# Performance work log

Measured on AMD Instinct MI355X. Metric: run time of the kernel, lower is better.

The kernel has to match this reference:

```python
import jax, jax.numpy as jnp
import numpy as np

N = 100000
E = 1600000
IN_C = 128
OUT_C = 64
HID = 2 * OUT_C  # 128


def setup_inputs() -> dict:
    key = jax.random.key(0)
    ks = jax.random.split(key, 10)
    s = lambda fan_in: 1.0 / np.sqrt(fan_in)
    inp = {
        "x": jax.random.normal(ks[0], (N, IN_C), dtype=jnp.float32),
        "edge_index": jax.random.randint(ks[1], (2, E), 0, N, dtype=jnp.int64),
        # SAGEConv params: lin_l acts on aggregated neighbors (with bias), lin_r on root (no bias)
        "W1l": jax.random.uniform(ks[2], (IN_C, HID), jnp.float32, -s(IN_C), s(IN_C)),
        "b1": jnp.zeros((HID,), jnp.float32),
        "W1r": jax.random.uniform(ks[3], (IN_C, HID), jnp.float32, -s(IN_C), s(IN_C)),
        "Wml": jax.random.uniform(ks[4], (HID, OUT_C), jnp.float32, -s(HID), s(HID)),
        "bm": jnp.zeros((OUT_C,), jnp.float32),
        "Wmr": jax.random.uniform(ks[5], (HID, OUT_C), jnp.float32, -s(HID), s(HID)),
        "Wsl": jax.random.uniform(ks[6], (HID, OUT_C), jnp.float32, -s(HID), s(HID)),
        "bs": jnp.zeros((OUT_C,), jnp.float32),
        "Wsr": jax.random.uniform(ks[7], (HID, OUT_C), jnp.float32, -s(HID), s(HID)),
    }
    return inp


def _sage_mean(x, src, dst, Wl, b, Wr):
    n = x.shape[0]
    # mean aggregation of source features onto destination nodes
    agg = jax.ops.segment_sum(x[src], dst, num_segments=n)
    cnt = jax.ops.segment_sum(jnp.ones((src.shape[0],), x.dtype), dst, num_segments=n)
    agg = agg / jnp.maximum(cnt, 1.0)[:, None]
    return agg @ Wl + b + x @ Wr


def reference(x, edge_index, W1l, b1, W1r, Wml, bm, Wmr, Wsl, bs, Wsr):
    src, dst = edge_index[0], edge_index[1]
    h = jax.nn.relu(_sage_mean(x, src, dst, W1l, b1, W1r))
    mu = _sage_mean(h, src, dst, Wml, bm, Wmr)
    logstd = _sage_mean(h, src, dst, Wsl, bs, Wsr)
    return mu, logstd
```

## Files before the change

kernel.cpp:

```cpp
#include <hip/hip_runtime.h>


typedef __attribute__((ext_vector_type(8))) short bf16x8;
typedef __attribute__((ext_vector_type(4))) float f32x4;
typedef __attribute__((ext_vector_type(2))) float f32x2;

#define SHIFT 9
#define BW 512

__device__ __forceinline__ unsigned short f2bf(float f) {
    unsigned u = __builtin_bit_cast(unsigned, f);
    u += 0x7fff + ((u >> 16) & 1);
    return (unsigned short)(u >> 16);
}
__device__ __forceinline__ float bflo(unsigned u) { return __builtin_bit_cast(float, u << 16); }
__device__ __forceinline__ float bfhi(unsigned u) { return __builtin_bit_cast(float, u & 0xffff0000u); }

__global__ __launch_bounds__(256) void prep_kernel(
    const float* __restrict__ x, const int* __restrict__ raw, int* __restrict__ flag,
    const float* __restrict__ W1l, const float* __restrict__ W1r,
    const float* __restrict__ Wml, const float* __restrict__ Wmr,
    const float* __restrict__ Wsl, const float* __restrict__ Wsr,
    const float* __restrict__ bm, const float* __restrict__ bs,
    unsigned short* __restrict__ B1p, unsigned short* __restrict__ B2p,
    float* __restrict__ bc, unsigned short* __restrict__ A1,
    unsigned short* __restrict__ A2, int n, int nE, int nXB) {
    const int b = blockIdx.x;
    const int t = threadIdx.x;
    if (b < nXB) {
        int i = (b * 256 + t) * 4;
        if (i < n * 128) {
            float4 v = *reinterpret_cast<const float4*>(x + i);
            int row = i >> 7, col = i & 127;
            unsigned short* p = A1 + (size_t)row * 256 + 128 + col;
            p[0] = f2bf(v.x); p[1] = f2bf(v.y); p[2] = f2bf(v.z); p[3] = f2bf(v.w);
        }
    } else if (b < nXB + 64) {
        const int nCheck = nE < 65536 ? nE : 65536;
        int acc = 0;
        for (int i = (b - nXB) * 256 + t; i < nCheck; i += 64 * 256)
            acc |= raw[2 * i + 1];
        if (acc) atomicOr(flag, 1);
    } else if (b < nXB + 192) {
        int i = (b - nXB - 64) * 256 + t;
        int j = i & 7, lq = (i >> 3) & 63, ks = (i >> 9) & 7, nf = i >> 12;
        int k = ks * 32 + (lq >> 4) * 8 + j;
        int c = nf * 16 + (lq & 15);
        float w1 = (k < 128) ? W1l[k * 128 + c] : W1r[(k - 128) * 128 + c];
        float w2;
        if (k < 128) w2 = (c < 64) ? Wml[k * 64 + c] : Wsl[k * 64 + (c - 64)];
        else         w2 = (c < 64) ? Wmr[(k - 128) * 64 + c] : Wsr[(k - 128) * 64 + (c - 64)];
        B1p[i] = f2bf(w1);
        B2p[i] = f2bf(w2);
        if (i < 128) bc[i] = (i < 64) ? bm[i] : bs[i - 64];
    } else {
        if (t < 64) {
            ((unsigned*)A1)[(size_t)n * 128 + 64 + t] = 0;
            ((unsigned*)A2)[(size_t)n * 128 + 64 + t] = 0;
        }
    }
}

__global__ __launch_bounds__(256) void binA_kernel(
    const int* __restrict__ raw, const int* __restrict__ flag,
    int* __restrict__ bcnt, unsigned* __restrict__ recs, int nE, int cap) {
    __shared__ int cnt[256];
    __shared__ int gbase[256];
    const int t = threadIdx.x;
    const bool is64 = (flag[0] == 0);
    const long long base = (long long)blockIdx.x * 1024;
    cnt[t] = 0;
    __syncthreads();
    int packv[4], loff[4], bk[4];
#pragma unroll
    for (int k = 0; k < 4; ++k) {
        long long e = base + t + k * 256;
        bk[k] = -1;
        if (e < nE) {
            int s, d;
            if (is64) { s = raw[2 * e]; d = raw[2 * (nE + e)]; }
            else      { s = raw[e];     d = raw[nE + e]; }
            bk[k] = d >> SHIFT;
            packv[k] = (s << SHIFT) | (d & (BW - 1));
            loff[k] = atomicAdd(&cnt[bk[k]], 1);
        }
    }
    __syncthreads();
    {
        int c = cnt[t];
        gbase[t] = c ? atomicAdd(&bcnt[t], c) : 0;
    }
    __syncthreads();
#pragma unroll
    for (int k = 0; k < 4; ++k) {
        if (bk[k] >= 0) {
            int pos = gbase[bk[k]] + loff[k];
            if (pos < cap) recs[(size_t)bk[k] * cap + pos] = (unsigned)packv[k];
        }
    }
}

__global__ __launch_bounds__(256) void binB_kernel(
    const unsigned* __restrict__ recs, const int* __restrict__ bcnt,
    int* __restrict__ rowptrP, int* __restrict__ cnts,
    int* __restrict__ csr, int cap, int n, int NB) {
    __shared__ int sdeg[BW];
    __shared__ int scur[BW];
    __shared__ int ssum[256];
    const int b = blockIdx.x;
    const int t = threadIdx.x;
    const int node0 = b << SHIFT;

    int rawb = (t < NB) ? bcnt[t] : 0;
    ssum[t] = rawb;
    __syncthreads();
    for (int off = 1; off < 256; off <<= 1) {
        int val = (t >= off) ? ssum[t - off] : 0;
        __syncthreads();
        ssum[t] += val;
        __syncthreads();
    }
    const int base = ((b == 0) ? 0 : ssum[b - 1]) + b * 3 * BW;
    int cnt = bcnt[b];
    if (cnt > cap) cnt = cap;
    const unsigned* r = recs + (size_t)b * cap;
    __syncthreads();

    sdeg[t] = 0;
    sdeg[t + 256] = 0;
    __syncthreads();
    for (int i = t; i < cnt; i += 256) atomicAdd(&sdeg[r[i] & (BW - 1)], 1);
    __syncthreads();
    int d0 = sdeg[2 * t], d1 = sdeg[2 * t + 1];
    int p0 = (d0 + 3) & ~3, p1 = (d1 + 3) & ~3;
    int sum = p0 + p1;
    ssum[t] = sum;
    __syncthreads();
    for (int off = 1; off < 256; off <<= 1) {
        int val = (t >= off) ? ssum[t - off] : 0;
        __syncthreads();
        ssum[t] += val;
        __syncthreads();
    }
    int ex = ssum[t] - sum;
    scur[2 * t] = ex;
    scur[2 * t + 1] = ex + p0;
    __syncthreads();
#pragma unroll
    for (int q = 0; q < 2; ++q) {
        int i = 2 * t + q;
        int node = node0 + i;
        if (node < n) {
            rowptrP[node] = base + scur[i];
            cnts[node] = sdeg[i];
        }
    }
    __syncthreads();
    for (int i = t; i < cnt; i += 256) {
        unsigned rec = r[i];
        int pos = base + atomicAdd(&scur[rec & (BW - 1)], 1);
        csr[pos] = (int)(rec >> SHIFT);
    }
    __syncthreads();
#pragma unroll
    for (int q = 0; q < 2; ++q) {
        int i = 2 * t + q;
        int node = node0 + i;
        if (node < n) {
            int d = sdeg[i];
            int pad = (4 - (d & 3)) & 3;
            int st = base + scur[i];
            for (int k = 0; k < pad; ++k) csr[st + k] = n;
        }
    }
}

__global__ __launch_bounds__(256) void gather_kernel(const unsigned int* __restrict__ feat,
                                                     const int* __restrict__ rowptrP,
                                                     const int* __restrict__ cnts,
                                                     const int* __restrict__ csr,
                                                     unsigned int* __restrict__ agg, int n) {
    int wv = (blockIdx.x * 256 + threadIdx.x) >> 6;
    if (wv >= n) return;
    int lane = threadIdx.x & 63;
    int eg = lane >> 4;
    int c4 = (lane & 15) * 4;
    int beg = rowptrP[wv];
    int deg = cnts[wv];
    int endp = beg + ((deg + 3) & ~3);
    f32x2 a0 = (f32x2)(0.f), a1 = (f32x2)(0.f), a2 = (f32x2)(0.f), a3 = (f32x2)(0.f);
    int jb = beg;
    if (jb < endp) {
        int s = csr[jb + eg];
        uint4 v = *reinterpret_cast<const uint4*>(feat + (size_t)s * 128 + c4);
#pragma unroll 2
        for (jb += 4; jb < endp; jb += 4) {
            int s2 = csr[jb + eg];
            uint4 v2 = *reinterpret_cast<const uint4*>(feat + (size_t)s2 * 128 + c4);
            a0 += (f32x2){bflo(v.x), bfhi(v.x)};
            a1 += (f32x2){bflo(v.y), bfhi(v.y)};
            a2 += (f32x2){bflo(v.z), bfhi(v.z)};
            a3 += (f32x2){bflo(v.w), bfhi(v.w)};
            v = v2;
        }
        a0 += (f32x2){bflo(v.x), bfhi(v.x)};
        a1 += (f32x2){bflo(v.y), bfhi(v.y)};
        a2 += (f32x2){bflo(v.z), bfhi(v.z)};
        a3 += (f32x2){bflo(v.w), bfhi(v.w)};
    }
    float acc[8] = {a0.x, a0.y, a1.x, a1.y, a2.x, a2.y, a3.x, a3.y};
#pragma unroll
    for (int q = 0; q < 8; ++q) {
        acc[q] += __shfl_xor(acc[q], 16);
        acc[q] += __shfl_xor(acc[q], 32);
    }
    if (eg == 0) {
        float ic = 1.0f / fmaxf((float)deg, 1.0f);
        uint4 r;
        r.x = (unsigned)f2bf(acc[0] * ic) | ((unsigned)f2bf(acc[1] * ic) << 16);
        r.y = (unsigned)f2bf(acc[2] * ic) | ((unsigned)f2bf(acc[3] * ic) << 16);
        r.z = (unsigned)f2bf(acc[4] * ic) | ((unsigned)f2bf(acc[5] * ic) << 16);
        r.w = (unsigned)f2bf(acc[6] * ic) | ((unsigned)f2bf(acc[7] * ic) << 16);
        *reinterpret_cast<uint4*>(agg + (size_t)wv * 128 + c4) = r;
    }
}

template <int MODE>
__global__ __launch_bounds__(256) void mfma_gemm(const unsigned short* __restrict__ A,
                                                 const unsigned short* __restrict__ Bp,
                                                 const float* __restrict__ bias,
                                                 void* __restrict__ outp, int n) {
    const int tid = threadIdx.x;
    const int w = tid >> 6, l = tid & 63;
    const int lr = l & 15;
    const int lg = l >> 4;
    const int row0 = blockIdx.x * 128 + w * 32;

    f32x4 acc[2][8];
#pragma unroll
    for (int mf = 0; mf < 2; ++mf)
#pragma unroll
        for (int nf = 0; nf < 8; ++nf) acc[mf][nf] = (f32x4)(0.0f);

    int r0 = row0 + lr;       if (r0 > n - 1) r0 = n - 1;
    int r1 = row0 + 16 + lr;  if (r1 > n - 1) r1 = n - 1;
    const unsigned short* a0p = A + (size_t)r0 * 256 + lg * 8;
    const unsigned short* a1p = A + (size_t)r1 * 256 + lg * 8;
    const unsigned short* bp = Bp + (size_t)l * 8;

    for (int ks = 0; ks < 8; ++ks) {
        bf16x8 a0 = *reinterpret_cast<const bf16x8*>(a0p + ks * 32);
        bf16x8 a1 = *reinterpret_cast<const bf16x8*>(a1p + ks * 32);
#pragma unroll
        for (int nf = 0; nf < 8; ++nf) {
            bf16x8 b = *reinterpret_cast<const bf16x8*>(bp + ((nf * 8 + ks) << 9));
            acc[0][nf] = __builtin_amdgcn_mfma_f32_16x16x32_bf16(a0, b, acc[0][nf], 0, 0, 0);
            acc[1][nf] = __builtin_amdgcn_mfma_f32_16x16x32_bf16(a1, b, acc[1][nf], 0, 0, 0);
        }
    }

    float bv[8];
#pragma unroll
    for (int nf = 0; nf < 8; ++nf) bv[nf] = bias[nf * 16 + lr];

#pragma unroll
    for (int mf = 0; mf < 2; ++mf)
#pragma unroll
        for (int j = 0; j < 4; ++j) {
            int row = row0 + mf * 16 + lg * 4 + j;
            if (row >= n) continue;
#pragma unroll
            for (int nf = 0; nf < 8; ++nf) {
                int col = nf * 16 + lr;
                float v = acc[mf][nf][j] + bv[nf];
                if (MODE == 0) {
                    v = fmaxf(v, 0.0f);
                    ((unsigned short*)outp)[(size_t)row * 256 + 128 + col] = f2bf(v);
                } else {
                    float* o = (float*)outp;
                    if (col < 64) o[(size_t)row * 64 + col] = v;
                    else o[(size_t)n * 64 + (size_t)row * 64 + (col - 64)] = v;
                }
            }
        }
}

extern "C" void kernel_launch(void* const* d_in, const int* in_sizes, int n_in,
                              void* d_out, int out_size, void* d_ws, size_t ws_size,
                              hipStream_t stream) {
    const float* x = (const float*)d_in[0];
    const int* eidx_raw = (const int*)d_in[1];
    const float* W1l = (const float*)d_in[2];
    const float* b1 = (const float*)d_in[3];
    const float* W1r = (const float*)d_in[4];
    const float* Wml = (const float*)d_in[5];
    const float* bm = (const float*)d_in[6];
    const float* Wmr = (const float*)d_in[7];
    const float* Wsl = (const float*)d_in[8];
    const float* bs = (const float*)d_in[9];
    const float* Wsr = (const float*)d_in[10];
    float* out = (float*)d_out;

    const int n = in_sizes[0] / 128;
    const int nE = in_sizes[1] / 2;

    const int NB = ((n - 1) >> SHIFT) + 1;
    long long capll = (((long long)nE << SHIFT) / n) * 5 / 4 + 1024;
    const int cap = (int)((capll + 15) & ~15LL);
    const int csr_ints = nE + NB * 3 * BW + 64;

    char* ws = (char*)d_ws;
    const size_t a_bytes = (size_t)(n + 1) * 512;
    const size_t a1_off = 0;
    const size_t a2_off = a1_off + a_bytes;
    const size_t recs_off = a2_off;
    const size_t csr_off = a2_off + a_bytes;
    const size_t rowptr_off = csr_off + (size_t)csr_ints * 4;
    const size_t cnts_off = rowptr_off + (size_t)n * 4;
    const size_t bcnt_off = cnts_off + (size_t)n * 4;
    const size_t flag_off = bcnt_off + 1024;
    const size_t b1p_off = (flag_off + 4 + 255) & ~(size_t)255;
    const size_t b2p_off = b1p_off + 65536;
    const size_t bc_off = b2p_off + 65536;

    unsigned short* A1 = (unsigned short*)(ws + a1_off);
    unsigned short* A2 = (unsigned short*)(ws + a2_off);
    unsigned* recs = (unsigned*)(ws + recs_off);
    int* csr = (int*)(ws + csr_off);
    int* rowptrP = (int*)(ws + rowptr_off);
    int* cnts = (int*)(ws + cnts_off);
    int* bcnt = (int*)(ws + bcnt_off);
    int* flag = (int*)(ws + flag_off);
    unsigned short* B1p = (unsigned short*)(ws + b1p_off);
    unsigned short* B2p = (unsigned short*)(ws + b2p_off);
    float* bc = (float*)(ws + bc_off);

    hipMemsetAsync(bcnt, 0, 1024 + 4, stream);

    const int nXB = (n * 32 + 255) / 256;
    prep_kernel<<<nXB + 193, 256, 0, stream>>>(x, eidx_raw, flag, W1l, W1r, Wml, Wmr,
                                               Wsl, Wsr, bm, bs, B1p, B2p, bc, A1, A2,
                                               n, nE, nXB);

    binA_kernel<<<(nE + 1023) / 1024, 256, 0, stream>>>(eidx_raw, flag, bcnt, recs, nE, cap);
    binB_kernel<<<NB, 256, 0, stream>>>(recs, bcnt, rowptrP, cnts, csr, cap, n, NB);

    const int gather_blocks = (n * 64 + 255) / 256;
    const int gemm_blocks = (n + 127) / 128;

    gather_kernel<<<gather_blocks, 256, 0, stream>>>(
        (const unsigned int*)A1 + 64, rowptrP, cnts, csr, (unsigned int*)A1, n);
    mfma_gemm<0><<<gemm_blocks, 256, 0, stream>>>(A1, B1p, b1, A2, n);

    gather_kernel<<<gather_blocks, 256, 0, stream>>>(
        (const unsigned int*)A2 + 64, rowptrP, cnts, csr, (unsigned int*)A2, n);
    mfma_gemm<1><<<gemm_blocks, 256, 0, stream>>>(A2, B2p, bc, out, n);
}
```

Before: 287.9 us.

## Fuse edge binning into prep kernel with per-block dtype check; prefetch gather indices

Merges the prep and binA kernels into one launch. Each binning block detects int64 vs int32 edge indices on its own, so the global flag and its memory dependency go away. Binning now runs in two passes (count, then scatter) over 4096 edges per block, which rereads the edge data. The gather loop also prefetches the next CSR index one iteration ahead to shorten the dependent-load chain.

```diff
diff --git a/kernel.cpp b/kernel.cpp
--- a/kernel.cpp
+++ b/kernel.cpp
@@ -16,33 +16,60 @@
 __device__ __forceinline__ float bflo(unsigned u) { return __builtin_bit_cast(float, u << 16); }
 __device__ __forceinline__ float bfhi(unsigned u) { return __builtin_bit_cast(float, u & 0xffff0000u); }
 
-__global__ __launch_bounds__(256) void prep_kernel(
-    const float* __restrict__ x, const int* __restrict__ raw, int* __restrict__ flag,
+__global__ __launch_bounds__(256) void stage1_kernel(
+    const float* __restrict__ x, const int* __restrict__ raw,
     const float* __restrict__ W1l, const float* __restrict__ W1r,
     const float* __restrict__ Wml, const float* __restrict__ Wmr,
     const float* __restrict__ Wsl, const float* __restrict__ Wsr,
     const float* __restrict__ bm, const float* __restrict__ bs,
     unsigned short* __restrict__ B1p, unsigned short* __restrict__ B2p,
     float* __restrict__ bc, unsigned short* __restrict__ A1,
-    unsigned short* __restrict__ A2, int n, int nE, int nXB) {
+    unsigned short* __restrict__ A2, int* __restrict__ bcnt,
+    unsigned* __restrict__ recs, int n, int nE, int cap, int nBinA, int nXB) {
     const int b = blockIdx.x;
     const int t = threadIdx.x;
-    if (b < nXB) {
-        int i = (b * 256 + t) * 4;
+    if (b < nBinA) {
+        __shared__ int cnt[256];
+        __shared__ int cur[256];
+        __shared__ int gbase[256];
+        __shared__ int sflag;
+        const int e0 = b * 4096;
+        const int e1 = (e0 + 4096 < nE) ? e0 + 4096 : nE;
+        int acc = 0;
+        for (int e = e0 + t; e < e1; e += 256) acc |= raw[2 * e + 1];
+        if (t == 0) sflag = 0;
+        cnt[t] = 0;
+        cur[t] = 0;
+        __syncthreads();
+        if (acc) atomicOr(&sflag, 1);
+        __syncthreads();
+        const bool is64 = (sflag == 0);
+        for (int e = e0 + t; e < e1; e += 256) {
+            int d = is64 ? raw[2 * (nE + e)] : raw[nE + e];
+            atomicAdd(&cnt[d >> SHIFT], 1);
+        }
+        __syncthreads();
+        gbase[t] = cnt[t] ? atomicAdd(&bcnt[t], cnt[t]) : 0;
+        __syncthreads();
+        for (int e = e0 + t; e < e1; e += 256) {
+            int s, d;
+            if (is64) { s = raw[2 * e]; d = raw[2 * (nE + e)]; }
+            else      { s = raw[e];     d = raw[nE + e]; }
+            int bk = d >> SHIFT;
+            int pos = gbase[bk] + atomicAdd(&cur[bk], 1);
+            if (pos < cap)
+                recs[(size_t)bk * cap + pos] = ((unsigned)s << SHIFT) | (unsigned)(d & (BW - 1));
+        }
+    } else if (b < nBinA + nXB) {
+        int i = ((b - nBinA) * 256 + t) * 4;
         if (i < n * 128) {
             float4 v = *reinterpret_cast<const float4*>(x + i);
             int row = i >> 7, col = i & 127;
             unsigned short* p = A1 + (size_t)row * 256 + 128 + col;
             p[0] = f2bf(v.x); p[1] = f2bf(v.y); p[2] = f2bf(v.z); p[3] = f2bf(v.w);
         }
-    } else if (b < nXB + 64) {
-        const int nCheck = nE < 65536 ? nE : 65536;
-        int acc = 0;
-        for (int i = (b - nXB) * 256 + t; i < nCheck; i += 64 * 256)
-            acc |= raw[2 * i + 1];
-        if (acc) atomicOr(flag, 1);
-    } else if (b < nXB + 192) {
-        int i = (b - nXB - 64) * 256 + t;
+    } else if (b < nBinA + nXB + 128) {
+        int i = (b - nBinA - nXB) * 256 + t;
         int j = i & 7, lq = (i >> 3) & 63, ks = (i >> 9) & 7, nf = i >> 12;
         int k = ks * 32 + (lq >> 4) * 8 + j;
         int c = nf * 16 + (lq & 15);
@@ -61,45 +88,6 @@
     }
 }
 
-__global__ __launch_bounds__(256) void binA_kernel(
-    const int* __restrict__ raw, const int* __restrict__ flag,
-    int* __restrict__ bcnt, unsigned* __restrict__ recs, int nE, int cap) {
-    __shared__ int cnt[256];
-    __shared__ int gbase[256];
-    const int t = threadIdx.x;
-    const bool is64 = (flag[0] == 0);
-    const long long base = (long long)blockIdx.x * 1024;
-    cnt[t] = 0;
-    __syncthreads();
-    int packv[4], loff[4], bk[4];
-#pragma unroll
-    for (int k = 0; k < 4; ++k) {
-        long long e = base + t + k * 256;
-        bk[k] = -1;
-        if (e < nE) {
-            int s, d;
-            if (is64) { s = raw[2 * e]; d = raw[2 * (nE + e)]; }
-            else      { s = raw[e];     d = raw[nE + e]; }
-            bk[k] = d >> SHIFT;
-            packv[k] = (s << SHIFT) | (d & (BW - 1));
-            loff[k] = atomicAdd(&cnt[bk[k]], 1);
-        }
-    }
-    __syncthreads();
-    {
-        int c = cnt[t];
-        gbase[t] = c ? atomicAdd(&bcnt[t], c) : 0;
-    }
-    __syncthreads();
-#pragma unroll
-    for (int k = 0; k < 4; ++k) {
-        if (bk[k] >= 0) {
-            int pos = gbase[bk[k]] + loff[k];
-            if (pos < cap) recs[(size_t)bk[k] * cap + pos] = (unsigned)packv[k];
-        }
-    }
-}
-
 __global__ __launch_bounds__(256) void binB_kernel(
     const unsigned* __restrict__ recs, const int* __restrict__ bcnt,
     int* __restrict__ rowptrP, int* __restrict__ cnts,
@@ -189,19 +177,22 @@
     int deg = cnts[wv];
     int endp = beg + ((deg + 3) & ~3);
     f32x2 a0 = (f32x2)(0.f), a1 = (f32x2)(0.f), a2 = (f32x2)(0.f), a3 = (f32x2)(0.f);
-    int jb = beg;
-    if (jb < endp) {
-        int s = csr[jb + eg];
-        uint4 v = *reinterpret_cast<const uint4*>(feat + (size_t)s * 128 + c4);
-#pragma unroll 2
-        for (jb += 4; jb < endp; jb += 4) {
-            int s2 = csr[jb + eg];
-            uint4 v2 = *reinterpret_cast<const uint4*>(feat + (size_t)s2 * 128 + c4);
+    if (deg > 0) {
+        int s0 = csr[beg + eg];
+        uint4 v = *reinterpret_cast<const uint4*>(feat + (size_t)s0 * 128 + c4);
+        int nx = beg + 4;
+        int s1 = csr[(nx < endp ? nx : beg) + eg];
+        while (nx < endp) {
+            uint4 v2 = *reinterpret_cast<const uint4*>(feat + (size_t)s1 * 128 + c4);
+            int nx2 = nx + 4;
+            int s2 = csr[(nx2 < endp ? nx2 : beg) + eg];
             a0 += (f32x2){bflo(v.x), bfhi(v.x)};
             a1 += (f32x2){bflo(v.y), bfhi(v.y)};
             a2 += (f32x2){bflo(v.z), bfhi(v.z)};
             a3 += (f32x2){bflo(v.w), bfhi(v.w)};
             v = v2;
+            s1 = s2;
+            nx = nx2;
         }
         a0 += (f32x2){bflo(v.x), bfhi(v.x)};
         a1 += (f32x2){bflo(v.y), bfhi(v.y)};
@@ -318,8 +309,7 @@
     const size_t rowptr_off = csr_off + (size_t)csr_ints * 4;
     const size_t cnts_off = rowptr_off + (size_t)n * 4;
     const size_t bcnt_off = cnts_off + (size_t)n * 4;
-    const size_t flag_off = bcnt_off + 1024;
-    const size_t b1p_off = (flag_off + 4 + 255) & ~(size_t)255;
+    const size_t b1p_off = (bcnt_off + 1024 + 255) & ~(size_t)255;
     const size_t b2p_off = b1p_off + 65536;
     const size_t bc_off = b2p_off + 65536;
 
@@ -330,19 +320,18 @@
     int* rowptrP = (int*)(ws + rowptr_off);
     int* cnts = (int*)(ws + cnts_off);
     int* bcnt = (int*)(ws + bcnt_off);
-    int* flag = (int*)(ws + flag_off);
     unsigned short* B1p = (unsigned short*)(ws + b1p_off);
     unsigned short* B2p = (unsigned short*)(ws + b2p_off);
     float* bc = (float*)(ws + bc_off);
 
-    hipMemsetAsync(bcnt, 0, 1024 + 4, stream);
-
+    hipMemsetAsync(bcnt, 0, 1024, stream);
+
+    const int nBinA = (nE + 4095) / 4096;
     const int nXB = (n * 32 + 255) / 256;
-    prep_kernel<<<nXB + 193, 256, 0, stream>>>(x, eidx_raw, flag, W1l, W1r, Wml, Wmr,
-                                               Wsl, Wsr, bm, bs, B1p, B2p, bc, A1, A2,
-                                               n, nE, nXB);
-
-    binA_kernel<<<(nE + 1023) / 1024, 256, 0, stream>>>(eidx_raw, flag, bcnt, recs, nE, cap);
+    stage1_kernel<<<nBinA + nXB + 129, 256, 0, stream>>>(
+        x, eidx_raw, W1l, W1r, Wml, Wmr, Wsl, Wsr, bm, bs,
+        B1p, B2p, bc, A1, A2, bcnt, recs, n, nE, cap, nBinA, nXB);
+
     binB_kernel<<<NB, 256, 0, stream>>>(recs, bcnt, rowptrP, cnts, csr, cap, n, NB);
 
     const int gather_blocks = (n * 64 + 255) / 256;
```

New measurement: 269.0 us. 1.07x faster.
